# Optimization experiments

Hardware: AMD Instinct MI355X
Metric: run time of the kernel (lower is better)

## Reference

```python
import jax, jax.numpy as jnp
import numpy as np

FACTOR = 5  # sampling factor from __init__


def setup_inputs() -> dict:
    key = jax.random.key(0)
    k1, k2, k3, k4 = jax.random.split(key, 4)
    B, L, H, D = 4, 2048, 8, 64
    S = min(FACTOR * int(np.ceil(np.log(L))), L)  # U_part = 40
    return {
        "queries": jax.random.normal(k1, (B, L, H, D), jnp.float32),
        "keys": jax.random.normal(k2, (B, L, H, D), jnp.float32),
        "values": jax.random.normal(k3, (B, L, H, D), jnp.float32),
        "index_sample": jax.random.randint(k4, (L, S), 0, L, jnp.int32),
    }


def reference(queries, keys, values, index_sample):
    B, L_Q, H, D = queries.shape
    L_K = keys.shape[1]
    Q = jnp.transpose(queries, (0, 2, 1, 3))  # [B,H,L_Q,D]
    K = jnp.transpose(keys, (0, 2, 1, 3))     # [B,H,L_K,D]
    V = jnp.transpose(values, (0, 2, 1, 3))   # [B,H,L_K,D]

    u = min(FACTOR * int(np.ceil(np.log(L_Q))), L_Q)  # n_top

    # --- _prob_QK: sampled QK to score queries, then top-u query selection ---
    # K_sample[b,h,q,s,:] = K[b,h,index_sample[q,s],:]  -> [B,H,L_Q,S,D]
    K_sample = K[:, :, index_sample, :]
    Q_K_sample = jnp.einsum('bhqd,bhqsd->bhqs', Q, K_sample)  # [B,H,L_Q,S]
    M = Q_K_sample.max(-1) - Q_K_sample.sum(-1) / L_K         # sparsity measure
    _, M_top = jax.lax.top_k(M, u)                            # [B,H,u] query indices

    Q_reduce = jnp.take_along_axis(Q, M_top[..., None], axis=2)  # [B,H,u,D]
    scale = 1.0 / np.sqrt(D)
    scores = jnp.einsum('bhud,bhkd->bhuk', Q_reduce, K) * scale  # [B,H,u,L_K]

    # --- _update_context causal mask: rows are the FIRST u rows of the full
    # triu(L_Q,L_Q) mask (faithful to original, which does NOT reindex by M_top)
    causal = jnp.triu(jnp.ones((u, L_Q), dtype=bool), 1)
    scores = jnp.where(causal[None, None], -jnp.inf, scores)
    attn = jax.nn.softmax(scores, axis=-1)
    upd = jnp.einsum('bhuk,bhkd->bhud', attn, V)  # [B,H,u,D]

    # --- _get_initial_context (mask_flag=True): running cumsum of V ---
    context = jnp.cumsum(V, axis=2)  # [B,H,L_Q,D]

    # scatter-overwrite selected query positions
    b = jnp.arange(B)[:, None, None]
    h = jnp.arange(H)[None, :, None]
    context = context.at[b, h, M_top].set(upd)

    return jnp.transpose(context, (0, 2, 1, 3))  # [B,L_Q,H,D]
```

## Files before the change

kernel.cpp:

```cpp
#include <hip/hip_runtime.h>
#include <stdint.h>

constexpr int B = 4;
constexpr int L = 2048;
constexpr int H = 8;
constexpr int D = 64;
constexpr int S = 40;
constexpr int U = 40;
constexpr int HD = H * D;
constexpr int NSEG = 8;
constexpr int SEGL = L / NSEG;
constexpr int NC = 64;
constexpr int CL = L / NC;

__device__ __forceinline__ unsigned mono(float v) {
    unsigned u = __float_as_uint(v);
    return (u & 0x80000000u) ? ~u : (u | 0x80000000u);
}

__global__ __launch_bounds__(256) void k_scores(
    const float4* __restrict__ Q4, const float4* __restrict__ K4,
    const int* __restrict__ idxs, float* __restrict__ M, int* __restrict__ flags)
{
    int wave = blockIdx.x * 4 + (threadIdx.x >> 6);
    int lane = threadIdx.x & 63;
    int q  = wave & (L - 1);
    int bh = wave >> 11;
    int b = bh >> 3, h = bh & 7;
    int s_sub = lane >> 4;
    int d4 = lane & 15;

    float4 qv = Q4[((size_t)(b * L + q) * H + h) * 16 + d4];
    const int* ip = idxs + q * S;
    float mx = -INFINITY, sm = 0.f;
    #pragma unroll
    for (int t = 0; t < S / 4; ++t) {
        int ki = ip[t * 4 + s_sub];
        float4 kv = K4[((size_t)(b * L + ki) * H + h) * 16 + d4];
        float acc = qv.x * kv.x + qv.y * kv.y + qv.z * kv.z + qv.w * kv.w;
        acc += __shfl_xor(acc, 1);
        acc += __shfl_xor(acc, 2);
        acc += __shfl_xor(acc, 4);
        acc += __shfl_xor(acc, 8);
        mx = fmaxf(mx, acc);
        sm += acc;
    }
    mx = fmaxf(mx, __shfl_xor(mx, 16));
    mx = fmaxf(mx, __shfl_xor(mx, 32));
    sm += __shfl_xor(sm, 16);
    sm += __shfl_xor(sm, 32);

    if (lane == 0) {
        M[bh * L + q] = mx - sm * (1.0f / (float)L);
        flags[bh * L + q] = 0;
    }
}

__global__ __launch_bounds__(64) void k_seg_topk(
    const float* __restrict__ M, unsigned long long* __restrict__ cand)
{
    int blk = blockIdx.x;
    int bh = blk >> 3, seg = blk & 7;
    int lane = threadIdx.x;
    int j0 = seg * SEGL + lane * 4;

    float4 v = *(const float4*)(M + (size_t)bh * L + j0);
    unsigned m[4] = { mono(v.x), mono(v.y), mono(v.z), mono(v.w) };
    int rank[4] = { 0, 0, 0, 0 };

    #pragma unroll 4
    for (int src = 0; src < 64; ++src) {
        #pragma unroll
        for (int slot = 0; slot < 4; ++slot) {
            unsigned bm = __shfl(m[slot], src);
            int bj = src * 4 + slot;
            #pragma unroll
            for (int s = 0; s < 4; ++s) {
                int myj = lane * 4 + s;
                rank[s] += (bm > m[s]) || (bm == m[s] && bj < myj);
            }
        }
    }

    unsigned long long* out = cand + (size_t)blk * U;
    #pragma unroll
    for (int s = 0; s < 4; ++s)
        if (rank[s] < U)
            out[rank[s]] = ((unsigned long long)m[s] << 32)
                         | (unsigned)(~(unsigned)(j0 + s));
}

__global__ __launch_bounds__(256) void k_attn(
    const float4* __restrict__ Q4, const float4* __restrict__ K4,
    const float4* __restrict__ V4, const unsigned long long* __restrict__ cand,
    int* __restrict__ flags, float* __restrict__ upd)
{
    __shared__ unsigned long long cnd[NSEG * U];
    __shared__ int top_idx[U];
    __shared__ __align__(16) float Qs[U * 68];
    __shared__ __align__(16) float Ks[U * 68];
    __shared__ __align__(16) float Vs[U * 68];
    __shared__ float P[U * 41];

    int bh = blockIdx.x;
    int b = bh >> 3, h = bh & 7;
    int tid = threadIdx.x;

    for (int i = tid; i < NSEG * U; i += 256)
        cnd[i] = cand[(size_t)bh * NSEG * U + i];
    __syncthreads();

    {
        unsigned long long ka = cnd[tid < NSEG * U ? tid : 0];
        unsigned long long kb = (tid < NSEG * U - 256) ? cnd[256 + tid] : 0ULL;
        int ra = 0, rb = 0;
        for (int j = 0; j < NSEG * U; ++j) {
            unsigned long long kj = cnd[j];
            ra += (kj > ka);
            rb += (kj > kb);
        }
        if (tid < NSEG * U && ra < U) top_idx[ra] = (int)(~(unsigned)ka);
        if (tid < NSEG * U - 256 && rb < U) top_idx[rb] = (int)(~(unsigned)kb);
    }
    __syncthreads();

    if (tid < U) flags[bh * L + top_idx[tid]] = tid + 1;

    for (int i = tid; i < U * 16; i += 256) {
        int r = i >> 4, d4 = i & 15;
        size_t kvbase = ((size_t)(b * L + r) * H + h) * 16 + d4;
        *(float4*)(Ks + r * 68 + d4 * 4) = K4[kvbase];
        *(float4*)(Vs + r * 68 + d4 * 4) = V4[kvbase];
        *(float4*)(Qs + r * 68 + d4 * 4) =
            Q4[((size_t)(b * L + top_idx[r]) * H + h) * 16 + d4];
    }
    __syncthreads();

    const float scale = 0.125f;
    for (int p = tid; p < U * U; p += 256) {
        int r = p / U, k = p - r * U;
        if (k <= r) {
            float acc = 0.f;
            #pragma unroll
            for (int d = 0; d < D; d += 4) {
                float4 a = *(const float4*)(Qs + r * 68 + d);
                float4 c = *(const float4*)(Ks + k * 68 + d);
                acc += a.x * c.x + a.y * c.y + a.z * c.z + a.w * c.w;
            }
            P[r * 41 + k] = acc * scale;
        }
    }
    __syncthreads();

    if (tid < U) {
        int r = tid;
        float mval = -INFINITY;
        for (int k = 0; k <= r; ++k) mval = fmaxf(mval, P[r * 41 + k]);
        float ssum = 0.f;
        for (int k = 0; k <= r; ++k) {
            float e = expf(P[r * 41 + k] - mval);
            P[r * 41 + k] = e;
            ssum += e;
        }
        float inv = 1.f / ssum;
        for (int k = 0; k <= r; ++k) P[r * 41 + k] *= inv;
    }
    __syncthreads();

    for (int t = tid; t < U * D; t += 256) {
        int r = t >> 6, d = t & 63;
        for (; r < U; r += 4) {
            float acc = 0.f;
            for (int k = 0; k <= r; ++k) acc += P[r * 41 + k] * Vs[k * 68 + d];
            upd[((size_t)bh * U + r) * D + d] = acc;
        }
        break;
    }
}

__global__ __launch_bounds__(512) void k_chunksum(
    const float* __restrict__ V, float* __restrict__ partial)
{
    int b = blockIdx.x >> 6;
    int c = blockIdx.x & 63;
    int hd = threadIdx.x;
    const float* vp = V + ((size_t)(b * L + c * CL)) * HD + hd;
    float s = 0.f;
    #pragma unroll
    for (int l = 0; l < CL; ++l) s += vp[(size_t)l * HD];
    partial[((size_t)b * NC + c) * HD + hd] = s;
}

__global__ __launch_bounds__(512) void k_cumsum_out(
    const float* __restrict__ V, const float* __restrict__ partial,
    const int* __restrict__ flags, const float* __restrict__ upd,
    float* __restrict__ out)
{
    int b = blockIdx.x >> 6;
    int c = blockIdx.x & 63;
    int hd = threadIdx.x;
    int h = hd >> 6, d = hd & 63;

    float acc = 0.f;
    for (int cc = 0; cc < c; ++cc)
        acc += partial[((size_t)b * NC + cc) * HD + hd];

    const float* vp = V + ((size_t)(b * L + c * CL)) * HD + hd;
    float*       op = out + ((size_t)(b * L + c * CL)) * HD + hd;
    const int*   fp = flags + (b * H + h) * L + c * CL;
    const float* up = upd + (size_t)(b * H + h) * U * D + d;

    #pragma unroll 4
    for (int l = 0; l < CL; ++l) {
        acc += vp[(size_t)l * HD];
        int f = fp[l];
        op[(size_t)l * HD] = f ? up[(size_t)(f - 1) * D] : acc;
    }
}

extern "C" void kernel_launch(void* const* d_in, const int* in_sizes, int n_in,
                              void* d_out, int out_size, void* d_ws, size_t ws_size,
                              hipStream_t stream)
{
    const float* Q   = (const float*)d_in[0];
    const float* K   = (const float*)d_in[1];
    const float* V   = (const float*)d_in[2];
    const int*  idxs = (const int*)d_in[3];
    float* out = (float*)d_out;

    char* ws = (char*)d_ws;
    float* M       = (float*)(ws);
    int*   flags   = (int*)  (ws + 262144);
    float* upd     = (float*)(ws + 524288);
    float* partial = (float*)(ws + 851968);
    unsigned long long* cand = (unsigned long long*)(ws + 1376256);

    k_scores    <<<B * H * L / 4, 256, 0, stream>>>((const float4*)Q, (const float4*)K, idxs, M, flags);
    k_seg_topk  <<<B * H * NSEG,   64, 0, stream>>>(M, cand);
    k_attn      <<<B * H,         256, 0, stream>>>((const float4*)Q, (const float4*)K, (const float4*)V,
                                                    cand, flags, upd);
    k_chunksum  <<<B * NC,        512, 0, stream>>>(V, partial);
    k_cumsum_out<<<B * NC,        512, 0, stream>>>(V, partial, flags, upd, out);
}
```

Before: 189.9 us.

## Process all heads per wave in score kernel and prescan chunk partials

```diff
diff --git a/kernel.cpp b/kernel.cpp
--- a/kernel.cpp
+++ b/kernel.cpp
@@ -20,49 +20,52 @@
 
 __global__ __launch_bounds__(256) void k_scores(
     const float4* __restrict__ Q4, const float4* __restrict__ K4,
-    const int* __restrict__ idxs, float* __restrict__ M, int* __restrict__ flags)
-{
-    int wave = blockIdx.x * 4 + (threadIdx.x >> 6);
+    const int* __restrict__ idxs, float* __restrict__ M)
+{
+    int i = blockIdx.x;
+    int xcd = i & 7;
+    int b = xcd >> 1;
+    int qc = (i >> 3) * 2 + (xcd & 1);
+    int w = threadIdx.x >> 6;
     int lane = threadIdx.x & 63;
-    int q  = wave & (L - 1);
-    int bh = wave >> 11;
-    int b = bh >> 3, h = bh & 7;
-    int s_sub = lane >> 4;
-    int d4 = lane & 15;
-
-    float4 qv = Q4[((size_t)(b * L + q) * H + h) * 16 + d4];
-    const int* ip = idxs + q * S;
+    int q = qc * 4 + w;
+    int h = lane >> 3;
+    int dd = lane & 7;
+
+    const float4* qrow = Q4 + (size_t)(b * L + q) * 128;
+    float4 qa = qrow[2 * lane], qb = qrow[2 * lane + 1];
+
+    int v_idx = idxs[q * S + (lane < S ? lane : 0)];
+
+    const float4* kbase = K4 + (size_t)b * L * 128;
     float mx = -INFINITY, sm = 0.f;
-    #pragma unroll
-    for (int t = 0; t < S / 4; ++t) {
-        int ki = ip[t * 4 + s_sub];
-        float4 kv = K4[((size_t)(b * L + ki) * H + h) * 16 + d4];
-        float acc = qv.x * kv.x + qv.y * kv.y + qv.z * kv.z + qv.w * kv.w;
-        acc += __shfl_xor(acc, 1);
-        acc += __shfl_xor(acc, 2);
-        acc += __shfl_xor(acc, 4);
-        acc += __shfl_xor(acc, 8);
-        mx = fmaxf(mx, acc);
-        sm += acc;
-    }
-    mx = fmaxf(mx, __shfl_xor(mx, 16));
-    mx = fmaxf(mx, __shfl_xor(mx, 32));
-    sm += __shfl_xor(sm, 16);
-    sm += __shfl_xor(sm, 32);
-
-    if (lane == 0) {
-        M[bh * L + q] = mx - sm * (1.0f / (float)L);
-        flags[bh * L + q] = 0;
-    }
+    #pragma unroll 8
+    for (int s = 0; s < S; ++s) {
+        int ki = __shfl(v_idx, s);
+        const float4* krow = kbase + (size_t)ki * 128;
+        float4 ka = krow[2 * lane], kb = krow[2 * lane + 1];
+        float d = qa.x * ka.x + qa.y * ka.y + qa.z * ka.z + qa.w * ka.w
+                + qb.x * kb.x + qb.y * kb.y + qb.z * kb.z + qb.w * kb.w;
+        d += __shfl_xor(d, 1);
+        d += __shfl_xor(d, 2);
+        d += __shfl_xor(d, 4);
+        mx = fmaxf(mx, d);
+        sm += d;
+    }
+    if (dd == 0)
+        M[(b * 8 + h) * L + q] = mx - sm * (1.0f / (float)L);
 }
 
 __global__ __launch_bounds__(64) void k_seg_topk(
-    const float* __restrict__ M, unsigned long long* __restrict__ cand)
+    const float* __restrict__ M, unsigned long long* __restrict__ cand,
+    int* __restrict__ flags)
 {
     int blk = blockIdx.x;
     int bh = blk >> 3, seg = blk & 7;
     int lane = threadIdx.x;
     int j0 = seg * SEGL + lane * 4;
+
+    *(int4*)(flags + (size_t)bh * L + j0) = make_int4(0, 0, 0, 0);
 
     float4 v = *(const float4*)(M + (size_t)bh * L + j0);
     unsigned m[4] = { mono(v.x), mono(v.y), mono(v.z), mono(v.w) };
@@ -169,12 +172,9 @@
 
     for (int t = tid; t < U * D; t += 256) {
         int r = t >> 6, d = t & 63;
-        for (; r < U; r += 4) {
-            float acc = 0.f;
-            for (int k = 0; k <= r; ++k) acc += P[r * 41 + k] * Vs[k * 68 + d];
-            upd[((size_t)bh * U + r) * D + d] = acc;
-        }
-        break;
+        float acc = 0.f;
+        for (int k = 0; k <= r; ++k) acc += P[r * 41 + k] * Vs[k * 68 + d];
+        upd[((size_t)bh * U + r) * D + d] = acc;
     }
 }
 
@@ -191,6 +191,20 @@
     partial[((size_t)b * NC + c) * HD + hd] = s;
 }
 
+__global__ __launch_bounds__(512) void k_scan(float* __restrict__ partial)
+{
+    int b = blockIdx.x;
+    int hd = threadIdx.x;
+    float acc = 0.f;
+    #pragma unroll 8
+    for (int c = 0; c < NC; ++c) {
+        size_t o = ((size_t)b * NC + c) * HD + hd;
+        float v = partial[o];
+        partial[o] = acc;
+        acc += v;
+    }
+}
+
 __global__ __launch_bounds__(512) void k_cumsum_out(
     const float* __restrict__ V, const float* __restrict__ partial,
     const int* __restrict__ flags, const float* __restrict__ upd,
@@ -201,9 +215,7 @@
     int hd = threadIdx.x;
     int h = hd >> 6, d = hd & 63;
 
-    float acc = 0.f;
-    for (int cc = 0; cc < c; ++cc)
-        acc += partial[((size_t)b * NC + cc) * HD + hd];
+    float acc = partial[((size_t)b * NC + c) * HD + hd];
 
     const float* vp = V + ((size_t)(b * L + c * CL)) * HD + hd;
     float*       op = out + ((size_t)(b * L + c * CL)) * HD + hd;
@@ -235,10 +247,11 @@
     float* partial = (float*)(ws + 851968);
     unsigned long long* cand = (unsigned long long*)(ws + 1376256);
 
-    k_scores    <<<B * H * L / 4, 256, 0, stream>>>((const float4*)Q, (const float4*)K, idxs, M, flags);
-    k_seg_topk  <<<B * H * NSEG,   64, 0, stream>>>(M, cand);
-    k_attn      <<<B * H,         256, 0, stream>>>((const float4*)Q, (const float4*)K, (const float4*)V,
-                                                    cand, flags, upd);
-    k_chunksum  <<<B * NC,        512, 0, stream>>>(V, partial);
-    k_cumsum_out<<<B * NC,        512, 0, stream>>>(V, partial, flags, upd, out);
-}
+    k_scores    <<<B * L / 4,    256, 0, stream>>>((const float4*)Q, (const float4*)K, idxs, M);
+    k_seg_topk  <<<B * H * NSEG,  64, 0, stream>>>(M, cand, flags);
+    k_attn      <<<B * H,        256, 0, stream>>>((const float4*)Q, (const float4*)K, (const float4*)V,
+                                                   cand, flags, upd);
+    k_chunksum  <<<B * NC,       512, 0, stream>>>(V, partial);
+    k_scan      <<<B,            512, 0, stream>>>(partial);
+    k_cumsum_out<<<B * NC,       512, 0, stream>>>(V, partial, flags, upd, out);
+}
```

Result: faster. 174.3 us (-8.2%).
